# Kernel optimization log

Hardware: AMD Instinct MI355X
Metric: run time of the kernel (lower is better)

Reference implementation:

```python
import jax, jax.numpy as jnp
import numpy as np

NEG_SLOPE = 0.2  # PyG GATConv default leaky_relu slope


def gat_layer(x, src, dst, W, a_src, a_dst, n_nodes, heads, ch):
    # x: [N, in_dim]; W: [in_dim, heads*ch]
    h = (x @ W).reshape(n_nodes, heads, ch)              # [N, H, C]
    e_s = jnp.einsum('nhc,hc->nh', h, a_src)             # [N, H]
    e_d = jnp.einsum('nhc,hc->nh', h, a_dst)             # [N, H]
    e = jax.nn.leaky_relu(e_s[src] + e_d[dst], NEG_SLOPE)  # [E, H]
    # segment softmax over incoming edges of each destination node
    m = jax.lax.stop_gradient(jax.ops.segment_max(e, dst, num_segments=n_nodes))
    w = jnp.exp(e - m[dst])                              # [E, H]
    z = jax.ops.segment_sum(w, dst, num_segments=n_nodes)  # [N, H]
    alpha = w / z[dst]                                   # [E, H]
    msg = h[src] * alpha[:, :, None]                     # [E, H, C]
    out = jax.ops.segment_sum(msg, dst, num_segments=n_nodes)  # [N, H, C]
    return out


def setup_inputs() -> dict:
    key = jax.random.key(0)
    ks = jax.random.split(key, 12)
    N, E, D, H = 50000, 800000, 128, 4
    x = jax.random.normal(ks[0], (N, D), dtype=jnp.float32)
    edge_index = jax.random.randint(ks[1], (2, E), 0, N, dtype=jnp.int64)
    s1 = 1.0 / np.sqrt(D)
    s2 = 1.0 / np.sqrt(D * H)
    W1 = jax.random.normal(ks[2], (D, H * D), dtype=jnp.float32) * s1
    a1_src = jax.random.normal(ks[3], (H, D), dtype=jnp.float32) * s1
    a1_dst = jax.random.normal(ks[4], (H, D), dtype=jnp.float32) * s1
    b1 = jax.random.normal(ks[5], (H * D,), dtype=jnp.float32) * 0.01
    W2 = jax.random.normal(ks[6], (H * D, D), dtype=jnp.float32) * s2
    a2_src = jax.random.normal(ks[7], (1, D), dtype=jnp.float32) * s1
    a2_dst = jax.random.normal(ks[8], (1, D), dtype=jnp.float32) * s1
    b2 = jax.random.normal(ks[9], (D,), dtype=jnp.float32) * 0.01
    fc_w = jax.random.normal(ks[10], (D, 1), dtype=jnp.float32) * s1
    fc_b = jax.random.normal(ks[11], (1,), dtype=jnp.float32) * 0.01
    return {"x": x, "edge_index": edge_index, "W1": W1, "a1_src": a1_src,
            "a1_dst": a1_dst, "b1": b1, "W2": W2, "a2_src": a2_src,
            "a2_dst": a2_dst, "b2": b2, "fc_w": fc_w, "fc_b": fc_b}


def reference(x, edge_index, W1, a1_src, a1_dst, b1, W2, a2_src, a2_dst, b2, fc_w, fc_b):
    N, D = x.shape
    H = a1_src.shape[0]
    # add self-loops (PyG GATConv default add_self_loops=True)
    loop = jnp.arange(N, dtype=edge_index.dtype)
    src = jnp.concatenate([edge_index[0], loop])
    dst = jnp.concatenate([edge_index[1], loop])
    # conv1: heads=4, concat=True -> [N, H*D]
    h1 = gat_layer(x, src, dst, W1, a1_src, a1_dst, N, H, D)
    h1 = jax.nn.relu(h1.reshape(N, H * D) + b1)
    # dropout p=0.2 is identity in eval mode
    # conv2: heads=1 -> [N, D]
    h2 = gat_layer(h1, src, dst, W2, a2_src, a2_dst, N, 1, D)
    h2 = h2.reshape(N, D) + b2
    return h2 @ fc_w + fc_b  # [N, 1]
```

## Files before the change

kernel.cpp:

```cpp
#include <hip/hip_runtime.h>
#include <cstdint>
#include <cstddef>

constexpr int kN   = 50000;
constexpr int kE   = 800000;
constexpr int kEt  = kE + kN;
constexpr float kSlope = 0.2f;
constexpr int kScanB = (kN + 255) / 256;
constexpr int kConvB = (kN * 16 + 255) / 256;
constexpr int kHistB = (kEt + 255) / 256;

typedef __attribute__((ext_vector_type(8))) short bf8_t;
typedef __attribute__((ext_vector_type(4))) float f4_t;
typedef __attribute__((ext_vector_type(2))) float f2_t;

__device__ __align__(16) unsigned short g_xb[(size_t)kN * 128];
__device__ __align__(16) unsigned short g_aggx[(size_t)kN * 512];
__device__ __align__(16) unsigned short g_w1t[4 * 128 * 128];
__device__ __align__(16) float g_u[3][512];
__device__ __align__(16) float g_es1[kN * 4];
__device__ __align__(16) float g_ed1[kN * 4];
__device__ __align__(16) float2 g_sp[kN];
__device__ float g_ed2[kN];
__device__ float g_c0;
__device__ __align__(16) float g_p1s[4 * 128];
__device__ __align__(16) float g_p1d[4 * 128];
__device__ int g_deg[kN];
__device__ int g_ptr[kN + 1];
__device__ int g_cur[kN];
__device__ int g_srcs[kEt];
__device__ int g_bsum[kScanB];

__device__ __forceinline__ float lrelu(float x) { return x > 0.f ? x : kSlope * x; }

__device__ __forceinline__ bf8_t bf8_zero() {
  uint4 z = make_uint4(0u, 0u, 0u, 0u);
  return *(bf8_t*)&z;
}

__device__ __forceinline__ unsigned short f2bf1(float v) {
  unsigned u = __float_as_uint(v);
  unsigned r = (u + 0x7FFFu + ((u >> 16) & 1u)) >> 16;
  return (unsigned short)r;
}

__global__ __launch_bounds__(256) void k_init(const float* __restrict__ x,
    const int* __restrict__ ei,
    const float* __restrict__ W1, const float* __restrict__ W2,
    const float* __restrict__ a1s, const float* __restrict__ a1d,
    const float* __restrict__ a2s, const float* __restrict__ a2d,
    const float* __restrict__ b2, const float* __restrict__ fcw,
    const float* __restrict__ fcb) {
  const int b = blockIdx.x, t = threadIdx.x;
  if (b < 197) {
    int i = b * 256 + t;
    if (i < kN) {
      g_sp[i] = make_float2(0.f, 0.f);
      g_ed2[i] = 0.f;
    }
  } else if (b < 453) {
    int gid = (b - 197) * 256 + t;
    int h = gid >> 14, rem = gid & 16383;
    int c = rem >> 7, j = rem & 127;
    float v = W1[(size_t)c * 512 + h * 128 + j];
    g_w1t[((size_t)h * 128 + j) * 128 + c] = f2bf1(v);
  } else if (b < 457) {
    int gid = (b - 453) * 256 + t;
    int which = gid >> 9, idx = gid & 511;
    int h = idx >> 7, k = idx & 127;
    const float* a = which ? a1d : a1s;
    const float* wrow = W1 + (size_t)k * 512 + h * 128;
    float s = 0.f;
#pragma unroll 8
    for (int c = 0; c < 128; ++c) s += wrow[c] * a[h * 128 + c];
    (which ? g_p1d : g_p1s)[idx] = s;
  } else if (b < 463) {
    int gid = (b - 457) * 256 + t;
    if (gid < 1536) {
      int v = gid >> 9, k = gid & 511;
      const float* vv = v == 0 ? a2s : v == 1 ? a2d : fcw;
      const float* wrow = W2 + (size_t)k * 128;
      float s = 0.f;
#pragma unroll 8
      for (int c = 0; c < 128; ++c) s += wrow[c] * vv[c];
      g_u[v][k] = s;
    }
  } else if (b < 464) {
    if (t < 64) {
      float s = b2[t] * fcw[t] + b2[64 + t] * fcw[64 + t];
#pragma unroll
      for (int off = 32; off > 0; off >>= 1) s += __shfl_down(s, off);
      if (t == 0) g_c0 = s + fcb[0];
    }
  } else if (b < 464 + kConvB) {
    int g = (b - 464) * 256 + t;
    if (g < kN * 16) {
      const float* xp = x + (size_t)g * 8;
      float4 f0 = *(const float4*)xp;
      float4 f1 = *(const float4*)(xp + 4);
      unsigned w0 = (unsigned)f2bf1(f0.x) | ((unsigned)f2bf1(f0.y) << 16);
      unsigned w1 = (unsigned)f2bf1(f0.z) | ((unsigned)f2bf1(f0.w) << 16);
      unsigned w2 = (unsigned)f2bf1(f1.x) | ((unsigned)f2bf1(f1.y) << 16);
      unsigned w3 = (unsigned)f2bf1(f1.z) | ((unsigned)f2bf1(f1.w) << 16);
      *(uint4*)(g_xb + (size_t)g * 8) = make_uint4(w0, w1, w2, w3);
    }
  } else {
    int e = (b - 464 - kConvB) * 256 + t;
    if (e < kEt) {
      int d = (e < kE) ? ei[kE + e] : e - kE;
      atomicAdd(&g_deg[d], 1);
    }
  }
}

__global__ __launch_bounds__(256) void k_scanA() {
  __shared__ int s[256];
  const int b = blockIdx.x, t = threadIdx.x;
  const int i = b * 256 + t;
  int d = (i < kN) ? g_deg[i] : 0;
  s[t] = d;
  __syncthreads();
  for (int off = 1; off < 256; off <<= 1) {
    int v = s[t];
    int u = (t >= off) ? s[t - off] : 0;
    __syncthreads();
    s[t] = v + u;
    __syncthreads();
  }
  if (t == 255) g_bsum[b] = s[255];
  if (i < kN) {
    g_ptr[i] = s[t] - d;
    g_deg[i] = 0;
  }
}

__global__ __launch_bounds__(256) void k_scanC() {
  __shared__ int s[256];
  const int b = blockIdx.x, t = threadIdx.x;
  int v = (t < kScanB) ? g_bsum[t] : 0;
  s[t] = v;
  __syncthreads();
  for (int off = 1; off < 256; off <<= 1) {
    int a = s[t];
    int u = (t >= off) ? s[t - off] : 0;
    __syncthreads();
    s[t] = a + u;
    __syncthreads();
  }
  const int boff = (b > 0) ? s[b - 1] : 0;
  __syncthreads();
  const int i = b * 256 + t;
  if (i < kN) {
    int p = g_ptr[i] + boff;
    g_ptr[i] = p;
    g_cur[i] = p;
  }
  if (b == 0 && t == 0) g_ptr[kN] = kEt;
}

__global__ __launch_bounds__(256) void k_scatter(const int* __restrict__ ei) {
  int e = blockIdx.x * 256 + threadIdx.x;
  if (e >= kEt) return;
  int s, d;
  if (e < kE) { s = ei[e]; d = ei[kE + e]; } else { s = d = e - kE; }
  int slot = atomicAdd(&g_cur[d], 1);
  g_srcs[slot] = s;
}

__global__ __launch_bounds__(256) void k_scores1x(const float* __restrict__ x) {
  const int lane = threadIdx.x & 63;
  const int n = (blockIdx.x * 256 + threadIdx.x) >> 6;
  if (n >= kN) return;
  float x0 = x[(size_t)n * 128 + lane];
  float x1 = x[(size_t)n * 128 + 64 + lane];
  float s[4], d[4];
#pragma unroll
  for (int h = 0; h < 4; ++h) {
    s[h] = x0 * g_p1s[h * 128 + lane] + x1 * g_p1s[h * 128 + 64 + lane];
    d[h] = x0 * g_p1d[h * 128 + lane] + x1 * g_p1d[h * 128 + 64 + lane];
  }
#pragma unroll
  for (int off = 32; off > 0; off >>= 1) {
#pragma unroll
    for (int h = 0; h < 4; ++h) {
      s[h] += __shfl_down(s[h], off);
      d[h] += __shfl_down(d[h], off);
    }
  }
  if (lane == 0) {
    *(float4*)(g_es1 + (size_t)n * 4) = make_float4(s[0], s[1], s[2], s[3]);
    *(float4*)(g_ed1 + (size_t)n * 4) = make_float4(d[0], d[1], d[2], d[3]);
  }
}

__global__ __launch_bounds__(256) void k_agg1x() {
  const int lane = threadIdx.x & 63;
  const int n = (blockIdx.x * 256 + threadIdx.x) >> 6;
  if (n >= kN) return;
  const int beg = g_ptr[n], end = g_ptr[n + 1];
  const float4 ed = *(const float4*)(g_ed1 + (size_t)n * 4);
  const int qt = lane >> 4, ql = lane & 15;
  float z0 = 0.f, z1 = 0.f, z2 = 0.f, z3 = 0.f;
  f2_t acc[4][4] = {};
  for (int base = beg; base < end; base += 64) {
    const int cnt = min(64, end - base);
    int s = 0;
    float w0 = 0.f, w1 = 0.f, w2 = 0.f, w3 = 0.f;
    if (lane < cnt) {
      s = g_srcs[base + lane];
      float4 es = *(const float4*)(g_es1 + (size_t)s * 4);
      w0 = __expf(lrelu(es.x + ed.x));
      w1 = __expf(lrelu(es.y + ed.y));
      w2 = __expf(lrelu(es.z + ed.z));
      w3 = __expf(lrelu(es.w + ed.w));
      z0 += w0; z1 += w1; z2 += w2; z3 += w3;
    }
    auto proc = [&](const uint4& uu, int e) {
      float b0 = __shfl(w0, e), b1 = __shfl(w1, e);
      float b2 = __shfl(w2, e), b3 = __shfl(w3, e);
      f2_t bb0 = b0, bb1 = b1, bb2 = b2, bb3 = b3;
      unsigned ws[4] = {uu.x, uu.y, uu.z, uu.w};
#pragma unroll
      for (int d = 0; d < 4; ++d) {
        f2_t fv;
        fv[0] = __uint_as_float(ws[d] << 16);
        fv[1] = __uint_as_float(ws[d] & 0xFFFF0000u);
        acc[0][d] += bb0 * fv;
        acc[1][d] += bb1 * fv;
        acc[2][d] += bb2 * fv;
        acc[3][d] += bb3 * fv;
      }
    };
    const int quads = (cnt + 3) >> 2;
    int p = 0;
    for (; p + 4 <= quads; p += 4) {
      const int e0 = 4 * p + qt;
      int sj0 = __shfl(s, e0);
      int sj1 = __shfl(s, e0 + 4);
      int sj2 = __shfl(s, e0 + 8);
      int sj3 = __shfl(s, e0 + 12);
      uint4 u0 = *(const uint4*)(g_xb + (size_t)sj0 * 128 + ql * 8);
      uint4 u1 = *(const uint4*)(g_xb + (size_t)sj1 * 128 + ql * 8);
      uint4 u2 = *(const uint4*)(g_xb + (size_t)sj2 * 128 + ql * 8);
      uint4 u3 = *(const uint4*)(g_xb + (size_t)sj3 * 128 + ql * 8);
      proc(u0, e0);
      proc(u1, e0 + 4);
      proc(u2, e0 + 8);
      proc(u3, e0 + 12);
    }
    for (; p < quads; ++p) {
      const int e = 4 * p + qt;
      int sj = __shfl(s, e);
      uint4 uu = *(const uint4*)(g_xb + (size_t)sj * 128 + ql * 8);
      proc(uu, e);
    }
  }
  const bool low = qt < 2;
  const bool ev = (qt & 1) == 0;
#pragma unroll
  for (int j = 0; j < 2; ++j)
#pragma unroll
    for (int d = 0; d < 4; ++d) {
      f2_t keep = low ? acc[j][d] : acc[j + 2][d];
      f2_t send = low ? acc[j + 2][d] : acc[j][d];
      f2_t r;
      r[0] = __shfl_xor(send[0], 32);
      r[1] = __shfl_xor(send[1], 32);
      acc[j][d] = keep + r;
    }
  f2_t res[4];
#pragma unroll
  for (int d = 0; d < 4; ++d) {
    f2_t keep = ev ? acc[0][d] : acc[1][d];
    f2_t send = ev ? acc[1][d] : acc[0][d];
    f2_t r;
    r[0] = __shfl_xor(send[0], 16);
    r[1] = __shfl_xor(send[1], 16);
    res[d] = keep + r;
  }
#pragma unroll
  for (int off = 1; off < 16; off <<= 1) {
    z0 += __shfl_xor(z0, off); z1 += __shfl_xor(z1, off);
    z2 += __shfl_xor(z2, off); z3 += __shfl_xor(z3, off);
  }
  float ka = low ? z0 : z2, kb = low ? z1 : z3;
  float sa = low ? z2 : z0, sb = low ? z3 : z1;
  ka += __shfl_xor(sa, 32);
  kb += __shfl_xor(sb, 32);
  float zh = (ev ? ka : kb) + __shfl_xor(ev ? kb : ka, 16);
  const float iz = 1.f / zh;
  unsigned wd[4];
#pragma unroll
  for (int d = 0; d < 4; ++d) {
    f2_t v = res[d] * iz;
    wd[d] = (unsigned)f2bf1(v[0]) | ((unsigned)f2bf1(v[1]) << 16);
  }
  *(uint4*)(g_aggx + (size_t)n * 512 + qt * 128 + ql * 8) =
      make_uint4(wd[0], wd[1], wd[2], wd[3]);
}

__global__ __launch_bounds__(256) void k_fused(const float* __restrict__ b1) {
  __shared__ float sred[2][64][3];
  const int t = threadIdx.x;
  const int lane = t & 63, w = t >> 6;
  const int wrow = w >> 1, wcol = w & 1;
  const int ln15 = lane & 15, q = lane >> 4, qo = q * 8;
  const int row0 = blockIdx.y * 64;
  const int h = blockIdx.z;

  float part[2][4][3] = {};
  f4_t h1acc[2][4] = {};
#pragma unroll
  for (int ks = 0; ks < 128; ks += 32) {
    bf8_t ah[2];
#pragma unroll
    for (int i = 0; i < 2; ++i) {
      int r = row0 + wrow * 32 + i * 16 + ln15;
      ah[i] = bf8_zero();
      if (r < kN)
        ah[i] = *(const bf8_t*)&g_aggx[(size_t)r * 512 + h * 128 + ks + qo];
    }
#pragma unroll
    for (int j = 0; j < 4; ++j) {
      size_t gb = ((size_t)h * 128 + wcol * 64 + j * 16 + ln15) * 128 + ks + qo;
      bf8_t bh = *(const bf8_t*)&g_w1t[gb];
#pragma unroll
      for (int i = 0; i < 2; ++i)
        h1acc[i][j] = __builtin_amdgcn_mfma_f32_16x16x32_bf16(ah[i], bh, h1acc[i][j], 0, 0, 0);
    }
  }
#pragma unroll
  for (int j = 0; j < 4; ++j) {
    int col = h * 128 + wcol * 64 + j * 16 + ln15;
    float bv = b1[col];
    float u0 = g_u[0][col], u1 = g_u[1][col], u2 = g_u[2][col];
#pragma unroll
    for (int i = 0; i < 2; ++i)
#pragma unroll
      for (int reg = 0; reg < 4; ++reg) {
        float v = fmaxf(h1acc[i][j][reg] + bv, 0.f);
        part[i][reg][0] += v * u0;
        part[i][reg][1] += v * u1;
        part[i][reg][2] += v * u2;
      }
  }
#pragma unroll
  for (int off = 1; off < 16; off <<= 1)
#pragma unroll
    for (int i = 0; i < 2; ++i)
#pragma unroll
      for (int reg = 0; reg < 4; ++reg)
#pragma unroll
        for (int v = 0; v < 3; ++v)
          part[i][reg][v] += __shfl_xor(part[i][reg][v], off);
  if (ln15 == 0) {
#pragma unroll
    for (int i = 0; i < 2; ++i)
#pragma unroll
      for (int reg = 0; reg < 4; ++reg) {
        int rl = wrow * 32 + i * 16 + q * 4 + reg;
#pragma unroll
        for (int v = 0; v < 3; ++v) sred[wcol][rl][v] = part[i][reg][v];
      }
  }
  __syncthreads();
  if (t < 192) {
    int row = t / 3, v = t - row * 3;
    float s = sred[0][row][v] + sred[1][row][v];
    int r = row0 + row;
    if (r < kN) {
      float* dst = v == 0 ? &g_sp[r].x : v == 1 ? &g_ed2[r] : &g_sp[r].y;
      atomicAdd(dst, s);
    }
  }
}

__global__ __launch_bounds__(256) void k_agg2s(float* __restrict__ out) {
  const int lane = threadIdx.x & 63;
  const int n = (blockIdx.x * 256 + threadIdx.x) >> 6;
  if (n >= kN) return;
  const int beg = g_ptr[n], end = g_ptr[n + 1];
  const float ed = g_ed2[n];
  float zp = 0.f, num = 0.f;
  for (int base = beg; base < end; base += 64) {
    int slot = base + lane;
    if (slot < end) {
      int s = g_srcs[slot];
      float2 sp = g_sp[s];
      float w = __expf(lrelu(sp.x + ed));
      zp += w;
      num += w * sp.y;
    }
  }
#pragma unroll
  for (int off = 1; off < 64; off <<= 1) {
    zp  += __shfl_xor(zp, off);
    num += __shfl_xor(num, off);
  }
  if (lane == 0) out[n] = num / zp + g_c0;
}

extern "C" void kernel_launch(void* const* d_in, const int* in_sizes, int n_in,
                              void* d_out, int out_size, void* d_ws, size_t ws_size,
                              hipStream_t stream) {
  const float* x   = (const float*)d_in[0];
  const int*   ei  = (const int*)d_in[1];
  const float* W1  = (const float*)d_in[2];
  const float* a1s = (const float*)d_in[3];
  const float* a1d = (const float*)d_in[4];
  const float* b1  = (const float*)d_in[5];
  const float* W2  = (const float*)d_in[6];
  const float* a2s = (const float*)d_in[7];
  const float* a2d = (const float*)d_in[8];
  const float* b2  = (const float*)d_in[9];
  const float* fcw = (const float*)d_in[10];
  const float* fcb = (const float*)d_in[11];
  float* out = (float*)d_out;
  (void)d_ws; (void)ws_size; (void)in_sizes; (void)n_in; (void)out_size;

  k_init<<<464 + kConvB + kHistB, 256, 0, stream>>>(x, ei, W1, W2, a1s, a1d,
                                                    a2s, a2d, b2, fcw, fcb);
  k_scanA<<<kScanB, 256, 0, stream>>>();
  k_scanC<<<kScanB, 256, 0, stream>>>();
  k_scatter<<<kHistB, 256, 0, stream>>>(ei);

  k_scores1x<<<(kN * 64 + 255) / 256, 256, 0, stream>>>(x);
  k_agg1x<<<(kN * 64 + 255) / 256, 256, 0, stream>>>();

  dim3 gf(1, (kN + 63) / 64, 4);
  k_fused<<<gf, 256, 0, stream>>>(b1);

  k_agg2s<<<(kN * 64 + 255) / 256, 256, 0, stream>>>(out);
}
```

Baseline: 319.2 us.

## Assign 16 lanes per node in aggregation kernels and fuse layer-1 scores into scan

The layer-1 aggregation and the layer-2 softmax aggregation now process four destination nodes per wavefront, 16 lanes each, instead of one node per 64-lane wave. With about 17 edges per node on average, most of a 64-lane wave sat idle, and the cross-quarter shuffle reduction was needed to combine partial sums. The layer-1 attention score computation is moved into extra blocks of the scan kernel, which removes one launch and overlaps it with the scan. The trade-off is less memory-level parallelism per node on high-degree nodes, and fewer outstanding gathers per lane, since the unroll is cut from 4 to 2.

```diff
diff --git a/kernel.cpp b/kernel.cpp
--- a/kernel.cpp
+++ b/kernel.cpp
@@ -9,6 +9,7 @@
 constexpr int kScanB = (kN + 255) / 256;
 constexpr int kConvB = (kN * 16 + 255) / 256;
 constexpr int kHistB = (kEt + 255) / 256;
+constexpr int kQuarB = (kN * 16 + 255) / 256;
 
 typedef __attribute__((ext_vector_type(8))) short bf8_t;
 typedef __attribute__((ext_vector_type(4))) float f4_t;
@@ -113,9 +114,46 @@
   }
 }
 
-__global__ __launch_bounds__(256) void k_scanA() {
+__device__ __forceinline__ void scores1_body(const float* __restrict__ x,
+                                             int bid, int t) {
+  const int lane = t & 63;
+  const int qt = lane >> 4, ql = lane & 15;
+  const int n = ((bid * 256 + t) >> 6) * 4 + qt;
+  if (n >= kN) return;
+  const float* xp = x + (size_t)n * 128 + ql * 8;
+  float4 xa = *(const float4*)xp;
+  float4 xb = *(const float4*)(xp + 4);
+  float s[4], d[4];
+#pragma unroll
+  for (int h = 0; h < 4; ++h) {
+    const float* ps = g_p1s + h * 128 + ql * 8;
+    const float* pd = g_p1d + h * 128 + ql * 8;
+    s[h] = xa.x * ps[0] + xa.y * ps[1] + xa.z * ps[2] + xa.w * ps[3]
+         + xb.x * ps[4] + xb.y * ps[5] + xb.z * ps[6] + xb.w * ps[7];
+    d[h] = xa.x * pd[0] + xa.y * pd[1] + xa.z * pd[2] + xa.w * pd[3]
+         + xb.x * pd[4] + xb.y * pd[5] + xb.z * pd[6] + xb.w * pd[7];
+  }
+#pragma unroll
+  for (int off = 1; off < 16; off <<= 1) {
+#pragma unroll
+    for (int h = 0; h < 4; ++h) {
+      s[h] += __shfl_xor(s[h], off);
+      d[h] += __shfl_xor(d[h], off);
+    }
+  }
+  if (ql == 0) {
+    *(float4*)(g_es1 + (size_t)n * 4) = make_float4(s[0], s[1], s[2], s[3]);
+    *(float4*)(g_ed1 + (size_t)n * 4) = make_float4(d[0], d[1], d[2], d[3]);
+  }
+}
+
+__global__ __launch_bounds__(256) void k_scanA(const float* __restrict__ x) {
   __shared__ int s[256];
   const int b = blockIdx.x, t = threadIdx.x;
+  if (b >= kScanB) {
+    scores1_body(x, b - kScanB, t);
+    return;
+  }
   const int i = b * 256 + t;
   int d = (i < kN) ? g_deg[i] : 0;
   s[t] = d;
@@ -167,47 +205,22 @@
   g_srcs[slot] = s;
 }
 
-__global__ __launch_bounds__(256) void k_scores1x(const float* __restrict__ x) {
-  const int lane = threadIdx.x & 63;
-  const int n = (blockIdx.x * 256 + threadIdx.x) >> 6;
-  if (n >= kN) return;
-  float x0 = x[(size_t)n * 128 + lane];
-  float x1 = x[(size_t)n * 128 + 64 + lane];
-  float s[4], d[4];
-#pragma unroll
-  for (int h = 0; h < 4; ++h) {
-    s[h] = x0 * g_p1s[h * 128 + lane] + x1 * g_p1s[h * 128 + 64 + lane];
-    d[h] = x0 * g_p1d[h * 128 + lane] + x1 * g_p1d[h * 128 + 64 + lane];
-  }
-#pragma unroll
-  for (int off = 32; off > 0; off >>= 1) {
-#pragma unroll
-    for (int h = 0; h < 4; ++h) {
-      s[h] += __shfl_down(s[h], off);
-      d[h] += __shfl_down(d[h], off);
-    }
-  }
-  if (lane == 0) {
-    *(float4*)(g_es1 + (size_t)n * 4) = make_float4(s[0], s[1], s[2], s[3]);
-    *(float4*)(g_ed1 + (size_t)n * 4) = make_float4(d[0], d[1], d[2], d[3]);
-  }
-}
-
 __global__ __launch_bounds__(256) void k_agg1x() {
   const int lane = threadIdx.x & 63;
-  const int n = (blockIdx.x * 256 + threadIdx.x) >> 6;
+  const int qt = lane >> 4, ql = lane & 15;
+  const int n = ((blockIdx.x * 256 + threadIdx.x) >> 6) * 4 + qt;
   if (n >= kN) return;
   const int beg = g_ptr[n], end = g_ptr[n + 1];
   const float4 ed = *(const float4*)(g_ed1 + (size_t)n * 4);
-  const int qt = lane >> 4, ql = lane & 15;
+  const int lbase = qt * 16;
   float z0 = 0.f, z1 = 0.f, z2 = 0.f, z3 = 0.f;
   f2_t acc[4][4] = {};
-  for (int base = beg; base < end; base += 64) {
-    const int cnt = min(64, end - base);
+  for (int base = beg; base < end; base += 16) {
+    const int cnt = min(16, end - base);
     int s = 0;
     float w0 = 0.f, w1 = 0.f, w2 = 0.f, w3 = 0.f;
-    if (lane < cnt) {
-      s = g_srcs[base + lane];
+    if (ql < cnt) {
+      s = g_srcs[base + ql];
       float4 es = *(const float4*)(g_es1 + (size_t)s * 4);
       w0 = __expf(lrelu(es.x + ed.x));
       w1 = __expf(lrelu(es.y + ed.y));
@@ -216,8 +229,8 @@
       z0 += w0; z1 += w1; z2 += w2; z3 += w3;
     }
     auto proc = [&](const uint4& uu, int e) {
-      float b0 = __shfl(w0, e), b1 = __shfl(w1, e);
-      float b2 = __shfl(w2, e), b3 = __shfl(w3, e);
+      float b0 = __shfl(w0, lbase + e), b1 = __shfl(w1, lbase + e);
+      float b2 = __shfl(w2, lbase + e), b3 = __shfl(w3, lbase + e);
       f2_t bb0 = b0, bb1 = b1, bb2 = b2, bb3 = b3;
       unsigned ws[4] = {uu.x, uu.y, uu.z, uu.w};
 #pragma unroll
@@ -231,72 +244,38 @@
         acc[3][d] += bb3 * fv;
       }
     };
-    const int quads = (cnt + 3) >> 2;
-    int p = 0;
-    for (; p + 4 <= quads; p += 4) {
-      const int e0 = 4 * p + qt;
-      int sj0 = __shfl(s, e0);
-      int sj1 = __shfl(s, e0 + 4);
-      int sj2 = __shfl(s, e0 + 8);
-      int sj3 = __shfl(s, e0 + 12);
+    int e = 0;
+    for (; e + 2 <= cnt; e += 2) {
+      int sj0 = __shfl(s, lbase + e);
+      int sj1 = __shfl(s, lbase + e + 1);
       uint4 u0 = *(const uint4*)(g_xb + (size_t)sj0 * 128 + ql * 8);
       uint4 u1 = *(const uint4*)(g_xb + (size_t)sj1 * 128 + ql * 8);
-      uint4 u2 = *(const uint4*)(g_xb + (size_t)sj2 * 128 + ql * 8);
-      uint4 u3 = *(const uint4*)(g_xb + (size_t)sj3 * 128 + ql * 8);
-      proc(u0, e0);
-      proc(u1, e0 + 4);
-      proc(u2, e0 + 8);
-      proc(u3, e0 + 12);
-    }
-    for (; p < quads; ++p) {
-      const int e = 4 * p + qt;
-      int sj = __shfl(s, e);
+      proc(u0, e);
+      proc(u1, e + 1);
+    }
+    if (e < cnt) {
+      int sj = __shfl(s, lbase + e);
       uint4 uu = *(const uint4*)(g_xb + (size_t)sj * 128 + ql * 8);
       proc(uu, e);
     }
-  }
-  const bool low = qt < 2;
-  const bool ev = (qt & 1) == 0;
-#pragma unroll
-  for (int j = 0; j < 2; ++j)
-#pragma unroll
-    for (int d = 0; d < 4; ++d) {
-      f2_t keep = low ? acc[j][d] : acc[j + 2][d];
-      f2_t send = low ? acc[j + 2][d] : acc[j][d];
-      f2_t r;
-      r[0] = __shfl_xor(send[0], 32);
-      r[1] = __shfl_xor(send[1], 32);
-      acc[j][d] = keep + r;
-    }
-  f2_t res[4];
-#pragma unroll
-  for (int d = 0; d < 4; ++d) {
-    f2_t keep = ev ? acc[0][d] : acc[1][d];
-    f2_t send = ev ? acc[1][d] : acc[0][d];
-    f2_t r;
-    r[0] = __shfl_xor(send[0], 16);
-    r[1] = __shfl_xor(send[1], 16);
-    res[d] = keep + r;
   }
 #pragma unroll
   for (int off = 1; off < 16; off <<= 1) {
     z0 += __shfl_xor(z0, off); z1 += __shfl_xor(z1, off);
     z2 += __shfl_xor(z2, off); z3 += __shfl_xor(z3, off);
   }
-  float ka = low ? z0 : z2, kb = low ? z1 : z3;
-  float sa = low ? z2 : z0, sb = low ? z3 : z1;
-  ka += __shfl_xor(sa, 32);
-  kb += __shfl_xor(sb, 32);
-  float zh = (ev ? ka : kb) + __shfl_xor(ev ? kb : ka, 16);
-  const float iz = 1.f / zh;
-  unsigned wd[4];
-#pragma unroll
-  for (int d = 0; d < 4; ++d) {
-    f2_t v = res[d] * iz;
-    wd[d] = (unsigned)f2bf1(v[0]) | ((unsigned)f2bf1(v[1]) << 16);
-  }
-  *(uint4*)(g_aggx + (size_t)n * 512 + qt * 128 + ql * 8) =
-      make_uint4(wd[0], wd[1], wd[2], wd[3]);
+  const float iz[4] = {1.f / z0, 1.f / z1, 1.f / z2, 1.f / z3};
+  const size_t nb = (size_t)n * 512 + ql * 8;
+#pragma unroll
+  for (int h = 0; h < 4; ++h) {
+    unsigned wd[4];
+#pragma unroll
+    for (int d = 0; d < 4; ++d) {
+      f2_t v = acc[h][d] * iz[h];
+      wd[d] = (unsigned)f2bf1(v[0]) | ((unsigned)f2bf1(v[1]) << 16);
+    }
+    *(uint4*)(g_aggx + nb + h * 128) = make_uint4(wd[0], wd[1], wd[2], wd[3]);
+  }
 }
 
 __global__ __launch_bounds__(256) void k_fused(const float* __restrict__ b1) {
@@ -377,27 +356,25 @@
 
 __global__ __launch_bounds__(256) void k_agg2s(float* __restrict__ out) {
   const int lane = threadIdx.x & 63;
-  const int n = (blockIdx.x * 256 + threadIdx.x) >> 6;
+  const int qt = lane >> 4, ql = lane & 15;
+  const int n = ((blockIdx.x * 256 + threadIdx.x) >> 6) * 4 + qt;
   if (n >= kN) return;
   const int beg = g_ptr[n], end = g_ptr[n + 1];
   const float ed = g_ed2[n];
   float zp = 0.f, num = 0.f;
-  for (int base = beg; base < end; base += 64) {
-    int slot = base + lane;
-    if (slot < end) {
-      int s = g_srcs[slot];
-      float2 sp = g_sp[s];
-      float w = __expf(lrelu(sp.x + ed));
-      zp += w;
-      num += w * sp.y;
-    }
-  }
-#pragma unroll
-  for (int off = 1; off < 64; off <<= 1) {
+  for (int slot = beg + ql; slot < end; slot += 16) {
+    int s = g_srcs[slot];
+    float2 sp = g_sp[s];
+    float w = __expf(lrelu(sp.x + ed));
+    zp += w;
+    num += w * sp.y;
+  }
+#pragma unroll
+  for (int off = 1; off < 16; off <<= 1) {
     zp  += __shfl_xor(zp, off);
     num += __shfl_xor(num, off);
   }
-  if (lane == 0) out[n] = num / zp + g_c0;
+  if (ql == 0) out[n] = num / zp + g_c0;
 }
 
 extern "C" void kernel_launch(void* const* d_in, const int* in_sizes, int n_in,
@@ -420,15 +397,14 @@
 
   k_init<<<464 + kConvB + kHistB, 256, 0, stream>>>(x, ei, W1, W2, a1s, a1d,
                                                     a2s, a2d, b2, fcw, fcb);
-  k_scanA<<<kScanB, 256, 0, stream>>>();
+  k_scanA<<<kScanB + kQuarB, 256, 0, stream>>>(x);
   k_scanC<<<kScanB, 256, 0, stream>>>();
   k_scatter<<<kHistB, 256, 0, stream>>>(ei);
 
-  k_scores1x<<<(kN * 64 + 255) / 256, 256, 0, stream>>>(x);
-  k_agg1x<<<(kN * 64 + 255) / 256, 256, 0, stream>>>();
+  k_agg1x<<<kQuarB, 256, 0, stream>>>();
 
   dim3 gf(1, (kN + 63) / 64, 4);
   k_fused<<<gf, 256, 0, stream>>>(b1);
 
-  k_agg2s<<<(kN * 64 + 255) / 256, 256, 0, stream>>>(out);
-}
+  k_agg2s<<<kQuarB, 256, 0, stream>>>(out);
+}
```

Result: faster. 292.1 us (-8.5%).
